# Kernel tuning notes

Hardware: AMD Instinct MI355X
Metric: run time of the kernel (lower is better)

The kernel has to match this reference:

```python
import jax, jax.numpy as jnp
import numpy as np

WIN_H, WIN_W, DILATION = 3, 3, 1
EPS = 1e-12  # torch F.normalize eps


def setup_inputs() -> dict:
    key = jax.random.key(0)
    feature = jax.random.normal(key, (4, 32, 256, 512), dtype=jnp.float32)
    return {"feature": feature}


def reference(feature):
    B, C, H, W = feature.shape
    d = DILATION
    # L2 normalize over channel dim (torch F.normalize semantics)
    norm = jnp.sqrt(jnp.sum(feature * feature, axis=1, keepdims=True))
    feat = feature / jnp.maximum(norm, EPS)
    # pad spatial dims by dilation (matches nn.Unfold padding=dilation for 3x3)
    padded = jnp.pad(feat, ((0, 0), (0, 0), (d, d), (d, d)))
    center_idx = (WIN_H * WIN_W) // 2
    affs = []
    # fixed small 3x3 stencil loop; each slice is a shifted view, dot with center
    for k in range(WIN_H * WIN_W):
        if k == center_idx:
            continue
        i, j = k // WIN_W, k % WIN_W
        nb = jax.lax.dynamic_slice(padded, (0, 0, i * d, j * d), (B, C, H, W))
        affs.append(jnp.sum(nb * feat, axis=1))  # (B,H,W)
    affinity = jnp.stack(affs, axis=1)  # (B, 8, H, W)
    cut = jnp.float32(0.0)
    return jnp.where(affinity < cut, cut, affinity)
```

## Files before the change

### kernel.cpp

```cpp
#include <hip/hip_runtime.h>


#define AF_B 4
#define AF_C 32
#define AF_H 256
#define AF_W 512
#define AF_EPS 1e-12f
#define AF_PLANE ((size_t)AF_H * AF_W)

#define LROW 72
#define LROWS 9
#define NSLOT 162

__global__ __launch_bounds__(256) void affinity_lds_kernel(const float* __restrict__ f,
                                                           float* __restrict__ out) {
    __shared__ float tile[2][LROWS][LROW];

    const int cpx = gridDim.x >> 3;
    const int bid = ((int)blockIdx.x & 7) * cpx + ((int)blockIdx.x >> 3);
    const int wband = bid & 7;
    const int hband = (bid >> 3) & 31;
    const int b = bid >> 8;

    const int h0 = hband << 3;
    const int wb0 = wband << 6;
    const int tid = (int)threadIdx.x;

    const int slot = tid;
    const int srow = slot / 18;
    const int scol4 = slot - srow * 18;
    const int gcol = wb0 + (scol4 << 2) - 4;
    const int grow = h0 + srow;
    const bool sv = (slot < NSLOT) && (gcol >= 0) && (gcol < AF_W) && (grow < AF_H);
    const size_t goff = (size_t)(sv ? grow : 0) * AF_W + (sv ? gcol : 0);
    const float* gsrc = f + (size_t)b * AF_C * AF_PLANE + goff;
    float* lslot0 = &tile[0][0][0] + (slot << 2);
    float* lslot1 = &tile[1][0][0] + (slot << 2);

    if (slot < NSLOT) {
        *(float4*)lslot0 = make_float4(0.f, 0.f, 0.f, 0.f);
        *(float4*)lslot1 = make_float4(0.f, 0.f, 0.f, 0.f);
    }
    if (sv) *(float4*)lslot0 = *(const float4*)gsrc;
    __syncthreads();

    const int g = tid & 31;
    const int r = tid >> 5;
    const int lcol = (g << 1) + 4;
    const int h = h0 + r;
    const int w0 = wb0 + (g << 1);

    float ssq0=0, ssq1=0, ssqR=0;
    float nsq0=0, nsq1=0, nsqL=0, nsqR=0;
    float dE0=0, dE1=0, dS0=0, dS1=0, dSE0=0, dSE1=0, dSW0=0, dSW1=0;

    const float* gnext = gsrc;
#pragma unroll 4
    for (int c = 0; c < AF_C; ++c) {
        float4 nx;
        const bool pf = sv && (c + 1 < AF_C);
        if (pf) { gnext += AF_PLANE; nx = *(const float4*)gnext; }

        const float (*cur)[LROW] = tile[c & 1];
        const float2 cc = *(const float2*)&cur[r][lcol];
        const float2 cs = *(const float2*)&cur[r + 1][lcol];
        const float ccR = cur[r][lcol + 2];
        const float csR = cur[r + 1][lcol + 2];
        const float csL = cur[r + 1][lcol - 1];

        ssq0 += cc.x*cc.x; ssq1 += cc.y*cc.y; ssqR += ccR*ccR;
        nsq0 += cs.x*cs.x; nsq1 += cs.y*cs.y; nsqL += csL*csL; nsqR += csR*csR;
        dE0  += cc.x*cc.y; dE1  += cc.y*ccR;
        dS0  += cc.x*cs.x; dS1  += cc.y*cs.y;
        dSE0 += cc.x*cs.y; dSE1 += cc.y*csR;
        dSW0 += cc.x*csL;  dSW1 += cc.y*cs.x;

        if (pf) *(float4*)((c & 1) ? lslot0 : lslot1) = nx;
        __syncthreads();
    }

    const float ic0 = 1.0f / fmaxf(sqrtf(ssq0), AF_EPS);
    const float ic1 = 1.0f / fmaxf(sqrtf(ssq1), AF_EPS);
    const float icR = 1.0f / fmaxf(sqrtf(ssqR), AF_EPS);
    const float is0 = 1.0f / fmaxf(sqrtf(nsq0), AF_EPS);
    const float is1 = 1.0f / fmaxf(sqrtf(nsq1), AF_EPS);
    const float isL = 1.0f / fmaxf(sqrtf(nsqL), AF_EPS);
    const float isR = 1.0f / fmaxf(sqrtf(nsqR), AF_EPS);

    const float E0  = fmaxf(dE0 *ic0*ic1, 0.0f);
    const float E1  = fmaxf(dE1 *ic1*icR, 0.0f);
    const float S0  = fmaxf(dS0 *ic0*is0, 0.0f);
    const float S1  = fmaxf(dS1 *ic1*is1, 0.0f);
    const float SE0 = fmaxf(dSE0*ic0*is1, 0.0f);
    const float SE1 = fmaxf(dSE1*ic1*isR, 0.0f);
    const float SW0 = fmaxf(dSW0*ic0*isL, 0.0f);
    const float SW1 = fmaxf(dSW1*ic1*is0, 0.0f);

    float* obase = out + (size_t)b * 8 * AF_PLANE + (size_t)h * AF_W + w0;
    const bool vR2 = (w0 + 2) < AF_W;
    const bool vL  = w0 > 0;
    const bool vS  = (h + 1) < AF_H;

    *(float2*)(obase + 4*AF_PLANE) = make_float2(E0, E1);
    *(float2*)(obase + 5*AF_PLANE) = make_float2(SW0, SW1);
    *(float2*)(obase + 6*AF_PLANE) = make_float2(S0, S1);
    *(float2*)(obase + 7*AF_PLANE) = make_float2(SE0, SE1);

    float* p3 = obase + 3*AF_PLANE;
    p3[1] = E0;
    if (vR2) p3[2] = E1;
    if (!vL) p3[0] = 0.0f;

    if (vS) {
        float* onb = obase + AF_W;
        *(float2*)(onb + 1*AF_PLANE) = make_float2(S0, S1);
        float* p0 = onb;
        p0[1] = SE0;
        if (vR2) p0[2] = SE1;
        if (!vL) p0[0] = 0.0f;
        float* p2 = onb + 2*AF_PLANE;
        if (vL) p2[-1] = SW0;
        p2[0] = SW1;
        if (!vR2) p2[1] = 0.0f;
    }

    if (h == 0) {
        float* oz = out + (size_t)b * 8 * AF_PLANE + w0;
        const float2 z2 = make_float2(0.0f, 0.0f);
        *(float2*)(oz + 0*AF_PLANE) = z2;
        *(float2*)(oz + 1*AF_PLANE) = z2;
        *(float2*)(oz + 2*AF_PLANE) = z2;
    }
}

extern "C" void kernel_launch(void* const* d_in, const int* in_sizes, int n_in,
                              void* d_out, int out_size, void* d_ws, size_t ws_size,
                              hipStream_t stream) {
    const float* f = (const float*)d_in[0];
    float* out = (float*)d_out;
    affinity_lds_kernel<<<1024, 256, 0, stream>>>(f, out);
}
```

Baseline: 24.01 us.

## Load eight channels per phase into LDS instead of per-channel double buffering

Each block now stages eight channel planes of its 9x72 halo tile into LDS per phase, using up to six float4 loads per thread issued together. It then accumulates over those eight channels with no barrier in between. This replaces the per-channel double-buffered pipeline with 32 barriers and raises the number of global loads in flight per block. In exchange, loads are no longer overlapped with compute inside a phase, and LDS use grows to about 20 KB per block, which may reduce occupancy.

```diff
diff --git a/kernel.cpp b/kernel.cpp
--- a/kernel.cpp
+++ b/kernel.cpp
@@ -10,11 +10,15 @@
 
 #define LROW 72
 #define LROWS 9
-#define NSLOT 162
+#define CHP 8
+#define NPHASE 4
+#define SLOTS_PER_CH 162
+#define SLOTS_PHASE (CHP * SLOTS_PER_CH)
+#define SITER 6
 
-__global__ __launch_bounds__(256) void affinity_lds_kernel(const float* __restrict__ f,
-                                                           float* __restrict__ out) {
-    __shared__ float tile[2][LROWS][LROW];
+__global__ __launch_bounds__(256) void affinity_bulk_kernel(const float* __restrict__ f,
+                                                            float* __restrict__ out) {
+    __shared__ float tile[CHP][LROWS][LROW];
 
     const int cpx = gridDim.x >> 3;
     const int bid = ((int)blockIdx.x & 7) * cpx + ((int)blockIdx.x >> 3);
@@ -26,23 +30,26 @@
     const int wb0 = wband << 6;
     const int tid = (int)threadIdx.x;
 
-    const int slot = tid;
-    const int srow = slot / 18;
-    const int scol4 = slot - srow * 18;
-    const int gcol = wb0 + (scol4 << 2) - 4;
-    const int grow = h0 + srow;
-    const bool sv = (slot < NSLOT) && (gcol >= 0) && (gcol < AF_W) && (grow < AF_H);
-    const size_t goff = (size_t)(sv ? grow : 0) * AF_W + (sv ? gcol : 0);
-    const float* gsrc = f + (size_t)b * AF_C * AF_PLANE + goff;
-    float* lslot0 = &tile[0][0][0] + (slot << 2);
-    float* lslot1 = &tile[1][0][0] + (slot << 2);
+    const float* fbase = f + (size_t)b * AF_C * AF_PLANE;
 
-    if (slot < NSLOT) {
-        *(float4*)lslot0 = make_float4(0.f, 0.f, 0.f, 0.f);
-        *(float4*)lslot1 = make_float4(0.f, 0.f, 0.f, 0.f);
+    int lofs[SITER];
+    const float* gptr[SITER];
+    bool act[SITER], val[SITER];
+#pragma unroll
+    for (int k = 0; k < SITER; ++k) {
+        const int slot = tid + (k << 8);
+        act[k] = slot < SLOTS_PHASE;
+        const int ch = slot / SLOTS_PER_CH;
+        const int rem = slot - ch * SLOTS_PER_CH;
+        const int srow = rem / 18;
+        const int sc4 = rem - srow * 18;
+        const int gcol = wb0 + (sc4 << 2) - 4;
+        const int grow = h0 + srow;
+        val[k] = act[k] && (gcol >= 0) && (gcol < AF_W) && (grow < AF_H);
+        lofs[k] = slot << 2;
+        gptr[k] = fbase + (size_t)ch * AF_PLANE
+                + (size_t)(val[k] ? grow : 0) * AF_W + (val[k] ? gcol : 0);
     }
-    if (sv) *(float4*)lslot0 = *(const float4*)gsrc;
-    __syncthreads();
 
     const int g = tid & 31;
     const int r = tid >> 5;
@@ -54,29 +61,37 @@
     float nsq0=0, nsq1=0, nsqL=0, nsqR=0;
     float dE0=0, dE1=0, dS0=0, dS1=0, dSE0=0, dSE1=0, dSW0=0, dSW1=0;
 
-    const float* gnext = gsrc;
-#pragma unroll 4
-    for (int c = 0; c < AF_C; ++c) {
-        float4 nx;
-        const bool pf = sv && (c + 1 < AF_C);
-        if (pf) { gnext += AF_PLANE; nx = *(const float4*)gnext; }
+    for (int p = 0; p < NPHASE; ++p) {
+        float4 v[SITER];
+        const size_t chofs = (size_t)p * CHP * AF_PLANE;
+#pragma unroll
+        for (int k = 0; k < SITER; ++k)
+            if (val[k]) v[k] = *(const float4*)(gptr[k] + chofs);
+#pragma unroll
+        for (int k = 0; k < SITER; ++k) {
+            if (val[k])
+                *(float4*)(&tile[0][0][0] + lofs[k]) = v[k];
+            else if (act[k] && p == 0)
+                *(float4*)(&tile[0][0][0] + lofs[k]) = make_float4(0.f,0.f,0.f,0.f);
+        }
+        __syncthreads();
 
-        const float (*cur)[LROW] = tile[c & 1];
-        const float2 cc = *(const float2*)&cur[r][lcol];
-        const float2 cs = *(const float2*)&cur[r + 1][lcol];
-        const float ccR = cur[r][lcol + 2];
-        const float csR = cur[r + 1][lcol + 2];
-        const float csL = cur[r + 1][lcol - 1];
+#pragma unroll
+        for (int c = 0; c < CHP; ++c) {
+            const float2 cc = *(const float2*)&tile[c][r][lcol];
+            const float2 cs = *(const float2*)&tile[c][r + 1][lcol];
+            const float ccR = tile[c][r][lcol + 2];
+            const float csR = tile[c][r + 1][lcol + 2];
+            const float csL = tile[c][r + 1][lcol - 1];
 
-        ssq0 += cc.x*cc.x; ssq1 += cc.y*cc.y; ssqR += ccR*ccR;
-        nsq0 += cs.x*cs.x; nsq1 += cs.y*cs.y; nsqL += csL*csL; nsqR += csR*csR;
-        dE0  += cc.x*cc.y; dE1  += cc.y*ccR;
-        dS0  += cc.x*cs.x; dS1  += cc.y*cs.y;
-        dSE0 += cc.x*cs.y; dSE1 += cc.y*csR;
-        dSW0 += cc.x*csL;  dSW1 += cc.y*cs.x;
-
-        if (pf) *(float4*)((c & 1) ? lslot0 : lslot1) = nx;
-        __syncthreads();
+            ssq0 += cc.x*cc.x; ssq1 += cc.y*cc.y; ssqR += ccR*ccR;
+            nsq0 += cs.x*cs.x; nsq1 += cs.y*cs.y; nsqL += csL*csL; nsqR += csR*csR;
+            dE0  += cc.x*cc.y; dE1  += cc.y*ccR;
+            dS0  += cc.x*cs.x; dS1  += cc.y*cs.y;
+            dSE0 += cc.x*cs.y; dSE1 += cc.y*csR;
+            dSW0 += cc.x*csL;  dSW1 += cc.y*cs.x;
+        }
+        if (p + 1 < NPHASE) __syncthreads();
     }
 
     const float ic0 = 1.0f / fmaxf(sqrtf(ssq0), AF_EPS);
@@ -138,5 +153,5 @@
                               hipStream_t stream) {
     const float* f = (const float*)d_in[0];
     float* out = (float*)d_out;
-    affinity_lds_kernel<<<1024, 256, 0, stream>>>(f, out);
+    affinity_bulk_kernel<<<1024, 256, 0, stream>>>(f, out);
 }
```

Result: slower. 44.81 us (+86.6%).

## Replace LDS double-buffered tile with direct per-thread global loads batched by channel

Applied to the files above, without the earlier changes.

Drops the shared-memory tile and its per-channel barriers. Each block now covers one full image row, and each thread reads its own center and south-row values straight from global memory, four channels at a time, so several loads are in flight at once. Boundary handling moves from zero-padded LDS to clamped offsets with multiplicative masks. Neighbouring-row and halo data are now re-fetched from global memory or L2 by different blocks and threads instead of being shared through LDS, so global traffic rises in exchange for removing the synchronization.

```diff
diff --git a/kernel.cpp b/kernel.cpp
--- a/kernel.cpp
+++ b/kernel.cpp
@@ -7,76 +7,63 @@
 #define AF_W 512
 #define AF_EPS 1e-12f
 #define AF_PLANE ((size_t)AF_H * AF_W)
+#define CB 4
 
-#define LROW 72
-#define LROWS 9
-#define NSLOT 162
-
-__global__ __launch_bounds__(256) void affinity_lds_kernel(const float* __restrict__ f,
-                                                           float* __restrict__ out) {
-    __shared__ float tile[2][LROWS][LROW];
-
+__global__ __launch_bounds__(256, 4) void affinity_reg_kernel(const float* __restrict__ f,
+                                                              float* __restrict__ out) {
     const int cpx = gridDim.x >> 3;
     const int bid = ((int)blockIdx.x & 7) * cpx + ((int)blockIdx.x >> 3);
-    const int wband = bid & 7;
-    const int hband = (bid >> 3) & 31;
+    const int h = bid & (AF_H - 1);
     const int b = bid >> 8;
 
-    const int h0 = hband << 3;
-    const int wb0 = wband << 6;
     const int tid = (int)threadIdx.x;
+    const int w0 = tid << 1;
 
-    const int slot = tid;
-    const int srow = slot / 18;
-    const int scol4 = slot - srow * 18;
-    const int gcol = wb0 + (scol4 << 2) - 4;
-    const int grow = h0 + srow;
-    const bool sv = (slot < NSLOT) && (gcol >= 0) && (gcol < AF_W) && (grow < AF_H);
-    const size_t goff = (size_t)(sv ? grow : 0) * AF_W + (sv ? gcol : 0);
-    const float* gsrc = f + (size_t)b * AF_C * AF_PLANE + goff;
-    float* lslot0 = &tile[0][0][0] + (slot << 2);
-    float* lslot1 = &tile[1][0][0] + (slot << 2);
+    const bool vR2 = (w0 + 2) < AF_W;
+    const bool vL  = w0 > 0;
+    const bool vS  = (h + 1) < AF_H;
+    const float mS  = vS ? 1.0f : 0.0f;
+    const float mR  = vR2 ? 1.0f : 0.0f;
+    const float mRS = mR * mS;
+    const float mLS = (vL ? 1.0f : 0.0f) * mS;
+    const int offR = vR2 ? 2 : 0;
+    const int offL = vL ? -1 : 0;
 
-    if (slot < NSLOT) {
-        *(float4*)lslot0 = make_float4(0.f, 0.f, 0.f, 0.f);
-        *(float4*)lslot1 = make_float4(0.f, 0.f, 0.f, 0.f);
-    }
-    if (sv) *(float4*)lslot0 = *(const float4*)gsrc;
-    __syncthreads();
-
-    const int g = tid & 31;
-    const int r = tid >> 5;
-    const int lcol = (g << 1) + 4;
-    const int h = h0 + r;
-    const int w0 = wb0 + (g << 1);
+    const float* pc = f + (size_t)b * AF_C * AF_PLANE + (size_t)h * AF_W + w0;
+    const float* ps = pc + (vS ? AF_W : 0);
 
     float ssq0=0, ssq1=0, ssqR=0;
     float nsq0=0, nsq1=0, nsqL=0, nsqR=0;
     float dE0=0, dE1=0, dS0=0, dS1=0, dSE0=0, dSE1=0, dSW0=0, dSW1=0;
 
-    const float* gnext = gsrc;
-#pragma unroll 4
-    for (int c = 0; c < AF_C; ++c) {
-        float4 nx;
-        const bool pf = sv && (c + 1 < AF_C);
-        if (pf) { gnext += AF_PLANE; nx = *(const float4*)gnext; }
+#pragma unroll
+    for (int gch = 0; gch < AF_C / CB; ++gch) {
+        float2 cc[CB], cs[CB];
+        float aR[CB], aL[CB], aRS[CB];
+#pragma unroll
+        for (int k = 0; k < CB; ++k) {
+            const float* p = pc + (size_t)(gch * CB + k) * AF_PLANE;
+            const float* q = ps + (size_t)(gch * CB + k) * AF_PLANE;
+            cc[k]  = *(const float2*)p;
+            aR[k]  = p[offR];
+            cs[k]  = *(const float2*)q;
+            aL[k]  = q[offL];
+            aRS[k] = q[offR];
+        }
+#pragma unroll
+        for (int k = 0; k < CB; ++k) {
+            const float ccx = cc[k].x, ccy = cc[k].y;
+            const float ccR = aR[k] * mR;
+            const float csx = cs[k].x * mS, csy = cs[k].y * mS;
+            const float csL = aL[k] * mLS, csR = aRS[k] * mRS;
 
-        const float (*cur)[LROW] = tile[c & 1];
-        const float2 cc = *(const float2*)&cur[r][lcol];
-        const float2 cs = *(const float2*)&cur[r + 1][lcol];
-        const float ccR = cur[r][lcol + 2];
-        const float csR = cur[r + 1][lcol + 2];
-        const float csL = cur[r + 1][lcol - 1];
-
-        ssq0 += cc.x*cc.x; ssq1 += cc.y*cc.y; ssqR += ccR*ccR;
-        nsq0 += cs.x*cs.x; nsq1 += cs.y*cs.y; nsqL += csL*csL; nsqR += csR*csR;
-        dE0  += cc.x*cc.y; dE1  += cc.y*ccR;
-        dS0  += cc.x*cs.x; dS1  += cc.y*cs.y;
-        dSE0 += cc.x*cs.y; dSE1 += cc.y*csR;
-        dSW0 += cc.x*csL;  dSW1 += cc.y*cs.x;
-
-        if (pf) *(float4*)((c & 1) ? lslot0 : lslot1) = nx;
-        __syncthreads();
+            ssq0 += ccx*ccx; ssq1 += ccy*ccy; ssqR += ccR*ccR;
+            nsq0 += csx*csx; nsq1 += csy*csy; nsqL += csL*csL; nsqR += csR*csR;
+            dE0  += ccx*ccy; dE1  += ccy*ccR;
+            dS0  += ccx*csx; dS1  += ccy*csy;
+            dSE0 += ccx*csy; dSE1 += ccy*csR;
+            dSW0 += ccx*csL; dSW1 += ccy*csx;
+        }
     }
 
     const float ic0 = 1.0f / fmaxf(sqrtf(ssq0), AF_EPS);
@@ -97,9 +84,6 @@
     const float SW1 = fmaxf(dSW1*ic1*is0, 0.0f);
 
     float* obase = out + (size_t)b * 8 * AF_PLANE + (size_t)h * AF_W + w0;
-    const bool vR2 = (w0 + 2) < AF_W;
-    const bool vL  = w0 > 0;
-    const bool vS  = (h + 1) < AF_H;
 
     *(float2*)(obase + 4*AF_PLANE) = make_float2(E0, E1);
     *(float2*)(obase + 5*AF_PLANE) = make_float2(SW0, SW1);
@@ -138,5 +122,5 @@
                               hipStream_t stream) {
     const float* f = (const float*)d_in[0];
     float* out = (float*)d_out;
-    affinity_lds_kernel<<<1024, 256, 0, stream>>>(f, out);
+    affinity_reg_kernel<<<1024, 256, 0, stream>>>(f, out);
 }
```

After: 27.45 us. 1.14x slower.
